# Kernel tuning notes

Hardware: AMD Instinct MI355X
Metric: run time of the kernel (lower is better)

The kernel has to match this reference:

```python
import math
import jax, jax.numpy as jnp
import numpy as np

L, NH, DF = 4, 4, 32  # num_layers, num_heads, head_dim (H=128)
EPS = 1e-5


def ln(x, g, b):
    m = x.mean(-1, keepdims=True)
    v = ((x - m) ** 2).mean(-1, keepdims=True)
    return (x - m) * jax.lax.rsqrt(v + EPS) * g + b


def mha(x, w_in, b_in, w_out, b_out):
    # torch nn.MultiheadAttention self-attention, batch_first, no mask
    B, S, H = x.shape
    q, k, v = jnp.split(x @ w_in + b_in, 3, axis=-1)
    q = q.reshape(B, S, NH, DF)
    k = k.reshape(B, S, NH, DF)
    v = v.reshape(B, S, NH, DF)
    s = jnp.einsum('bqhd,bkhd->bhqk', q, k) / math.sqrt(DF)
    a = jax.nn.softmax(s, axis=-1)
    o = jnp.einsum('bhqk,bkhd->bqhd', a, v).reshape(B, S, H)
    return o @ w_out + b_out


def _forward(X_k, time_embed, step_embed, W_tr, b_tr, W_in, b_in, g_in, be_in,
             W_e, b_e, aw, ab, ow, ob, tng, tnb, f1w, f1b, f2w, f2b, fng, fnb,
             Wq, Wk, Wv, Wo, bo, Wem, bem, Wea, bea, e1w, e1b, e2w, e2b,
             gng, gnb, eng, enb, W_out, b_out, k_index, edge_index):
    B, N, T1, Cin = X_k.shape
    H = W_in.shape[1]
    # --- precompute_graph: self-loops + structural edge features ---
    loop = jnp.arange(N, dtype=edge_index.dtype)
    ei = jnp.concatenate([edge_index, jnp.stack([loop, loop])], axis=1)
    dst, src = ei[0], ei[1]
    E = ei.shape[1]
    deg = jnp.zeros((N,), jnp.float32).at[dst].add(1.0)
    deg_max = jnp.maximum(deg.max(), 1.0)
    edge_w = 1.0 / jnp.maximum(deg[dst], 1.0)
    feat = jnp.stack([edge_w, deg[src] / deg_max, deg[dst] / deg_max], axis=1)  # [E,3]
    # --- input embedding ---
    t_emb = time_embed  # [T1, te] (lookup of arange(T1) = whole table)
    X = jnp.concatenate(
        [X_k, jnp.broadcast_to(t_emb[None, None], (B, N, T1, t_emb.shape[-1]))], axis=-1)
    h = ln(X @ W_in + b_in, g_in, be_in)
    h = h + step_embed[k_index][:, None, None, :]
    e = feat @ W_e + b_e                       # [E, de]
    t_re = t_emb @ W_tr + b_tr                 # [T1, H]
    BT = B * T1
    for l in range(L):
        # temporal attention over T1
        h_flat = h.reshape(B * N, T1, H)
        attn_out = mha(h_flat, aw[l], ab[l], ow[l], ob[l])
        h = ln(h + attn_out.reshape(B, N, T1, H), tng[l], tnb[l])
        ffn = jax.nn.gelu(h @ f1w[l] + f1b[l], approximate=False) @ f2w[l] + f2b[l]
        h = ln(h + ffn, fng[l], fnb[l])
        h = h + t_re[None, None]
        # DiGress GT sparse graph block over N
        h_BT = h.transpose(0, 2, 1, 3).reshape(BT, N, H)
        Q = (h_BT @ Wq[l]).reshape(BT, N, NH, DF)
        K = (h_BT @ Wk[l]).reshape(BT, N, NH, DF)
        V = (h_BT @ Wv[l]).reshape(BT, N, NH, DF)
        scores = (Q[:, dst] * K[:, src]).sum(-1) / math.sqrt(DF)  # [BT,E,NH]
        scores = scores * (e @ Wem[l] + bem[l] + 1.0) + (e @ Wea[l] + bea[l])
        s_max = jax.lax.stop_gradient(scores.max(axis=1, keepdims=True))
        exp_s = jnp.exp(scores - s_max)
        denom = jnp.zeros((BT, N, NH), exp_s.dtype).at[:, dst, :].add(exp_s)
        attn = exp_s / (denom[:, dst, :] + 1e-9)
        agg = (attn[..., None] * V[:, src]).reshape(BT, E, H)
        out = jnp.zeros((BT, N, H), h.dtype).at[:, dst, :].add(agg)
        h_BT = h_BT + out @ Wo[l] + bo[l]
        h_mean = jax.lax.stop_gradient(h_BT).mean(0)               # [N,H]
        e_in = jnp.concatenate([h_mean[dst], h_mean[src], e], axis=-1)
        e_mlp = jax.nn.gelu(e_in @ e1w[l] + e1b[l], approximate=False) @ e2w[l] + e2b[l]
        e = ln(e + e_mlp, eng[l], enb[l])
        h = ln(h_BT.reshape(B, T1, N, H).transpose(0, 2, 1, 3), gng[l], gnb[l])
    return jax.nn.softmax(h @ W_out + b_out, axis=-1)


def setup_inputs() -> dict:
    key = jax.random.key(0)
    B, N, T1 = 2, 2000, 12
    sd, cc, te, H, de, nh = 4, 2, 16, 128, 16, 4
    Cin = (1 + cc) * sd  # 12
    E0, max_steps = 32000, 1024
    ks = iter(jax.random.split(key, 60))
    def rn(*shape, s=0.05):
        return jax.random.normal(next(ks), shape, jnp.float32) * s
    z = lambda *s: jnp.zeros(s, jnp.float32)
    o = lambda *s: jnp.ones(s, jnp.float32)
    return dict(
        X_k=jax.random.normal(next(ks), (B, N, T1, Cin), jnp.float32),
        time_embed=rn(T1, te), step_embed=rn(max_steps, H),
        W_tr=rn(te, H), b_tr=z(H),
        W_in=rn(Cin + te, H), b_in=z(H), g_in=o(H), be_in=z(H),
        W_e=rn(3, de), b_e=z(de),
        aw=rn(L, H, 3 * H), ab=z(L, 3 * H), ow=rn(L, H, H), ob=z(L, H),
        tng=o(L, H), tnb=z(L, H),
        f1w=rn(L, H, 2 * H), f1b=z(L, 2 * H), f2w=rn(L, 2 * H, H), f2b=z(L, H),
        fng=o(L, H), fnb=z(L, H),
        Wq=rn(L, H, H), Wk=rn(L, H, H), Wv=rn(L, H, H),
        Wo=rn(L, H, H), bo=z(L, H),
        Wem=rn(L, de, nh), bem=z(L, nh), Wea=rn(L, de, nh), bea=z(L, nh),
        e1w=rn(L, 2 * H + de, 4 * de), e1b=z(L, 4 * de),
        e2w=rn(L, 4 * de, de), e2b=z(L, de),
        gng=o(L, H), gnb=z(L, H), eng=o(L, de), enb=z(L, de),
        W_out=rn(H, sd), b_out=z(sd),
        k_index=jax.random.randint(next(ks), (B,), 0, max_steps),
        edge_index=jax.random.randint(next(ks), (2, E0), 0, N),
    )


def reference(X_k, time_embed, step_embed, W_tr, b_tr, W_in, b_in, g_in, be_in,
              W_e, b_e, aw, ab, ow, ob, tng, tnb, f1w, f1b, f2w, f2b, fng, fnb,
              Wq, Wk, Wv, Wo, bo, Wem, bem, Wea, bea, e1w, e1b, e2w, e2b,
              gng, gnb, eng, enb, W_out, b_out, k_index, edge_index):
    return _forward(X_k, time_embed, step_embed, W_tr, b_tr, W_in, b_in, g_in, be_in,
                    W_e, b_e, aw, ab, ow, ob, tng, tnb, f1w, f1b, f2w, f2b, fng, fnb,
                    Wq, Wk, Wv, Wo, bo, Wem, bem, Wea, bea, e1w, e1b, e2w, e2b,
                    gng, gnb, eng, enb, W_out, b_out, k_index, edge_index)
```

## Files before the change

kernel.cpp:

```cpp
#include <hip/hip_runtime.h>
#include <math.h>

#define NN 2000
#define T1C 12
#define BBC 2
#define HHC 128
#define NHD 4
#define DFD 32
#define LLC 4
#define DEC 16
#define TEC 16
#define CINC 12
#define E0C 32000
#define EEC 34000
#define BTC 24
#define MROWS 48000
#define EPSLN 1e-5f
#define SCALEQK 0.17677669529663687f

typedef __attribute__((ext_vector_type(8))) short short8;
typedef __attribute__((ext_vector_type(4))) float f32x4;


__device__ __forceinline__ unsigned short f2b(float f)
{
    unsigned u = __float_as_uint(f);
    return (unsigned short)((u + 0x7FFF + ((u >> 16) & 1)) >> 16);
}

__device__ __forceinline__ float b2f(unsigned short h)
{
    return __uint_as_float(((unsigned)h) << 16);
}


__global__ __launch_bounds__(256) void convwp_k(const float* __restrict__ W, unsigned short* __restrict__ Bp,
                                                int LN_, int K, int N, int noff, int Ntot)
{
    int idx = blockIdx.x * blockDim.x + threadIdx.x;
    int total = LN_ * K * N;
    if (idx >= total) return;
    int l = idx / (K * N);
    int r = idx - l * (K * N);
    int k = r / N;
    int n = r - k * N + noff;
    size_t off = (size_t)l * K * Ntot +
                 ((size_t)((n >> 4) * (K >> 5) + (k >> 5)) << 9) +
                 (((k >> 3) & 3) << 7) + ((n & 15) << 3) + (k & 7);
    Bp[off] = f2b(W[idx]);
}

__global__ __launch_bounds__(256) void convw12_k(const float* __restrict__ e1w, unsigned short* __restrict__ W12P)
{
    int idx = blockIdx.x * blockDim.x + threadIdx.x;
    if (idx >= LLC * 128 * 128) return;
    int l = idx >> 14;
    int r = idx & 16383;
    int c = r >> 7, k = r & 127;
    int sk = (c < 64) ? k : k + 128;
    int sc = c & 63;
    W12P[idx] = f2b(e1w[((size_t)l * 272 + sk) * 64 + sc]);
}

__global__ __launch_bounds__(256) void convwoT_k(const float* __restrict__ Wo, unsigned short* __restrict__ WoT)
{
    int idx = blockIdx.x * blockDim.x + threadIdx.x;
    if (idx >= LLC * 128 * 128) return;
    int l = idx >> 14;
    int r = idx & 16383;
    int c = r >> 7, k = r & 127;
    WoT[idx] = f2b(Wo[((size_t)l * 128 + k) * 128 + c]);
}


template<int K, int EPI, int OUTM>
__global__ __launch_bounds__(256) void gemm2_k(
    const unsigned short* __restrict__ A, const unsigned short* __restrict__ Bp,
    const float* __restrict__ bias, float* __restrict__ C, unsigned short* __restrict__ Cb,
    const float* __restrict__ res, const float* __restrict__ gam, const float* __restrict__ bet,
    const float* __restrict__ trep,
    int M, int Ntot)
{
    __shared__ unsigned short A_s[128 * 16 * 8];
    __shared__ float red2[2][128][2];

    int tid = threadIdx.x;
    int w = tid >> 6, lane = tid & 63;
    int wr = w & 1, wc = w >> 1;
    int quad = lane >> 4, lr = lane & 15;

    const unsigned short* abase = A + (size_t)blockIdx.x * 128 * K;
    int ntg0 = blockIdx.y * 8 + wc * 4;

    f32x4 acc[4][4];
#pragma unroll
    for (int mt = 0; mt < 4; mt++)
#pragma unroll
        for (int nt = 0; nt < 4; nt++) acc[mt][nt] = (f32x4){0.f, 0.f, 0.f, 0.f};

#pragma unroll
    for (int kb = 0; kb < K; kb += 128) {
        if (kb) __syncthreads();
#pragma unroll
        for (int j = 0; j < 8; j++) {
            int s = j * 256 + tid;
            int row = s >> 4, ks = s & 15;
            int ko = ks ^ (row & 15);
            uint4 d = *(const uint4*)(abase + (size_t)row * K + kb + ko * 8);
            *(uint4*)(A_s + s * 8) = d;
        }
        __syncthreads();
#pragma unroll
        for (int k0 = 0; k0 < 128; k0 += 32) {
            short8 af[4], bf[4];
#pragma unroll
            for (int mt = 0; mt < 4; mt++) {
                int row_l = wr * 64 + mt * 16 + lr;
                int koct = (k0 >> 3) + quad;
                int slot = row_l * 16 + (koct ^ lr);
                af[mt] = *(const short8*)(A_s + slot * 8);
            }
#pragma unroll
            for (int nt = 0; nt < 4; nt++) {
                size_t off = ((size_t)(ntg0 + nt) * (K >> 5) + ((kb + k0) >> 5)) * 512 + lane * 8;
                bf[nt] = *(const short8*)(Bp + off);
            }
#pragma unroll
            for (int mt = 0; mt < 4; mt++)
#pragma unroll
                for (int nt = 0; nt < 4; nt++)
                    acc[mt][nt] = __builtin_amdgcn_mfma_f32_16x16x32_bf16(af[mt], bf[nt], acc[mt][nt], 0, 0, 0);
        }
    }

    int rbase = blockIdx.x * 128 + wr * 64;
    int cbase = blockIdx.y * 128 + wc * 64;

    if constexpr (EPI != 3 && EPI != 4 && EPI != 5) {
#pragma unroll
        for (int mt = 0; mt < 4; mt++) {
#pragma unroll
            for (int nt = 0; nt < 4; nt++) {
                int colg = cbase + nt * 16 + lr;
                float bv = bias ? bias[colg] : 0.f;
#pragma unroll
                for (int i = 0; i < 4; i++) {
                    int row = rbase + mt * 16 + quad * 4 + i;
                    float x = acc[mt][nt][i] + bv;
                    if constexpr (EPI == 1) x = 0.5f * x * (1.f + erff(x * 0.70710678118654752f));
                    if constexpr (EPI == 2) x = res[(size_t)row * Ntot + colg] + x;
                    if constexpr (OUTM & 1) C[(size_t)row * Ntot + colg] = x;
                    if constexpr (OUTM & 4)
                        Cb[(size_t)blockIdx.y * M * 128 + (size_t)row * 128 + (wc * 64 + nt * 16 + lr)] = f2b(x);
                    else if constexpr (OUTM & 2)
                        Cb[(size_t)row * Ntot + colg] = f2b(x);
                }
            }
        }
    } else {
        float s[4][4], s2l[4][4];
#pragma unroll
        for (int mt = 0; mt < 4; mt++)
#pragma unroll
            for (int i = 0; i < 4; i++) { s[mt][i] = 0.f; s2l[mt][i] = 0.f; }
#pragma unroll
        for (int mt = 0; mt < 4; mt++) {
#pragma unroll
            for (int nt = 0; nt < 4; nt++) {
                int colg = cbase + nt * 16 + lr;
                float bv = bias[colg];
#pragma unroll
                for (int i = 0; i < 4; i++) {
                    int row = rbase + mt * 16 + quad * 4 + i;
                    float x = acc[mt][nt][i] + bv + res[(size_t)row * 128 + colg];
                    acc[mt][nt][i] = x;
                    s[mt][i] += x;
                    s2l[mt][i] += x * x;
                }
            }
        }
#pragma unroll
        for (int m = 1; m < 16; m <<= 1) {
#pragma unroll
            for (int mt = 0; mt < 4; mt++)
#pragma unroll
                for (int i = 0; i < 4; i++) {
                    s[mt][i]  += __shfl_xor(s[mt][i], m, 64);
                    s2l[mt][i] += __shfl_xor(s2l[mt][i], m, 64);
                }
        }
        if (lr == 0) {
#pragma unroll
            for (int mt = 0; mt < 4; mt++)
#pragma unroll
                for (int i = 0; i < 4; i++) {
                    int rl = wr * 64 + mt * 16 + quad * 4 + i;
                    red2[wc][rl][0] = s[mt][i];
                    red2[wc][rl][1] = s2l[mt][i];
                }
        }
        __syncthreads();
#pragma unroll
        for (int mt = 0; mt < 4; mt++) {
#pragma unroll
            for (int i = 0; i < 4; i++) {
                int rl = wr * 64 + mt * 16 + quad * 4 + i;
                float st  = red2[0][rl][0] + red2[1][rl][0];
                float s2t = red2[0][rl][1] + red2[1][rl][1];
                float mu = st * (1.f / 128.f);
                float rstd = rsqrtf(s2t * (1.f / 128.f) - mu * mu + EPSLN);
                int row = rbase + mt * 16 + quad * 4 + i;
                if constexpr (EPI == 4) {
                    int t = row % T1C;
                    int bn = row / T1C;
                    int b = bn / NN;
                    int n = bn - b * NN;
                    size_t rowp = (size_t)(b * T1C + t) * NN + n;
                    const float* trow = trep + t * HHC;
#pragma unroll
                    for (int nt = 0; nt < 4; nt++) {
                        int colg = cbase + nt * 16 + lr;
                        float y = (acc[mt][nt][i] - mu) * rstd * gam[colg] + bet[colg] + trow[colg];
                        C[rowp * 128 + colg] = y;
                        Cb[rowp * 128 + colg] = f2b(y);
                    }
                } else if constexpr (EPI == 5) {
                    int bt = row / NN, n = row - bt * NN;
                    int b = bt / T1C, t = bt - b * T1C;
                    size_t rowp = ((size_t)(b * NN + n)) * T1C + t;
#pragma unroll
                    for (int nt = 0; nt < 4; nt++) {
                        int colg = cbase + nt * 16 + lr;
                        float y = (acc[mt][nt][i] - mu) * rstd * gam[colg] + bet[colg];
                        C[rowp * 128 + colg] = y;
                        Cb[rowp * 128 + colg] = f2b(y);
                    }
                } else {
#pragma unroll
                    for (int nt = 0; nt < 4; nt++) {
                        int colg = cbase + nt * 16 + lr;
                        float y = (acc[mt][nt][i] - mu) * rstd * gam[colg] + bet[colg];
                        if constexpr (OUTM & 1) C[(size_t)row * 128 + colg] = y;
                        if constexpr (OUTM & 2) Cb[(size_t)row * 128 + colg] = f2b(y);
                    }
                }
            }
        }
    }
}

template<int K, int EPI, int OUTM>
static void run_gemm2(const unsigned short* A, const unsigned short* Bp, const float* bias,
                      float* C, unsigned short* Cb, const float* res, const float* g, const float* be,
                      const float* trep, int M, int Ntot, hipStream_t stream)
{
    dim3 grid(M / 128, Ntot / 128);
    gemm2_k<K, EPI, OUTM><<<grid, 256, 0, stream>>>(A, Bp, bias, C, Cb, res, g, be, trep, M, Ntot);
}


__global__ __launch_bounds__(256) void ffn_k(
    const unsigned short* __restrict__ A,
    const unsigned short* __restrict__ F1p,
    const unsigned short* __restrict__ F2p,
    const float* __restrict__ f1b_l, const float* __restrict__ f2b_l,
    const float* __restrict__ res,
    const float* __restrict__ gam, const float* __restrict__ bet,
    const float* __restrict__ trep,
    float* __restrict__ C, unsigned short* __restrict__ Cb)
{
    __shared__ unsigned short A_s[32 * 16 * 8];
    __shared__ unsigned short M_s[32 * 16 * 8];
    __shared__ float red2[2][32][2];

    int tid = threadIdx.x;
    int w = tid >> 6, lane = tid & 63;
    int wr = w & 1, wc = w >> 1;
    int quad = lane >> 4, lr = lane & 15;

    const unsigned short* abase = A + (size_t)blockIdx.x * 32 * 128;

#pragma unroll
    for (int j = 0; j < 2; j++) {
        int s = j * 256 + tid;
        int row = s >> 4, ks = s & 15;
        int ko = ks ^ (row & 15);
        uint4 d = *(const uint4*)(abase + (size_t)row * 128 + ko * 8);
        *(uint4*)(A_s + s * 8) = d;
    }
    __syncthreads();

    f32x4 facc[4];
#pragma unroll
    for (int nt = 0; nt < 4; nt++) facc[nt] = (f32x4){0.f, 0.f, 0.f, 0.f};

#pragma unroll
    for (int half = 0; half < 2; half++) {
        f32x4 macc[4];
#pragma unroll
        for (int nt = 0; nt < 4; nt++) macc[nt] = (f32x4){0.f, 0.f, 0.f, 0.f};
#pragma unroll
        for (int k0 = 0; k0 < 128; k0 += 32) {
            int row_l = wr * 16 + lr;
            int koct = (k0 >> 3) + quad;
            int slot = row_l * 16 + (koct ^ lr);
            short8 af = *(const short8*)(A_s + slot * 8);
            short8 bf[4];
#pragma unroll
            for (int nt = 0; nt < 4; nt++) {
                size_t off = ((size_t)(half * 8 + wc * 4 + nt) * 4 + (k0 >> 5)) * 512 + lane * 8;
                bf[nt] = *(const short8*)(F1p + off);
            }
#pragma unroll
            for (int nt = 0; nt < 4; nt++)
                macc[nt] = __builtin_amdgcn_mfma_f32_16x16x32_bf16(af, bf[nt], macc[nt], 0, 0, 0);
        }
        if (half) __syncthreads();
#pragma unroll
        for (int nt = 0; nt < 4; nt++) {
            int col = wc * 64 + nt * 16 + lr;
            float bv = f1b_l[half * 128 + col];
            int cchunk = col >> 3, celem = col & 7;
#pragma unroll
            for (int i = 0; i < 4; i++) {
                int row = wr * 16 + quad * 4 + i;
                float x = macc[nt][i] + bv;
                x = 0.5f * x * (1.f + erff(x * 0.70710678118654752f));
                int ks = cchunk ^ (row & 15);
                M_s[(row * 16 + ks) * 8 + celem] = f2b(x);
            }
        }
        __syncthreads();
#pragma unroll
        for (int k0 = 0; k0 < 128; k0 += 32) {
            int row_l = wr * 16 + lr;
            int koct = (k0 >> 3) + quad;
            int slot = row_l * 16 + (koct ^ lr);
            short8 af = *(const short8*)(M_s + slot * 8);
            short8 bf[4];
#pragma unroll
            for (int nt = 0; nt < 4; nt++) {
                size_t off = ((size_t)(wc * 4 + nt) * 8 + ((half * 128 + k0) >> 5)) * 512 + lane * 8;
                bf[nt] = *(const short8*)(F2p + off);
            }
#pragma unroll
            for (int nt = 0; nt < 4; nt++)
                facc[nt] = __builtin_amdgcn_mfma_f32_16x16x32_bf16(af, bf[nt], facc[nt], 0, 0, 0);
        }
    }

    int rbase = blockIdx.x * 32 + wr * 16;
    int cbase = wc * 64;
    float s[4], s2l[4];
#pragma unroll
    for (int i = 0; i < 4; i++) { s[i] = 0.f; s2l[i] = 0.f; }
#pragma unroll
    for (int nt = 0; nt < 4; nt++) {
        int colg = cbase + nt * 16 + lr;
        float bv = f2b_l[colg];
#pragma unroll
        for (int i = 0; i < 4; i++) {
            int row = rbase + quad * 4 + i;
            float x = facc[nt][i] + bv + res[(size_t)row * 128 + colg];
            facc[nt][i] = x;
            s[i] += x;
            s2l[i] += x * x;
        }
    }
#pragma unroll
    for (int m = 1; m < 16; m <<= 1) {
#pragma unroll
        for (int i = 0; i < 4; i++) {
            s[i]  += __shfl_xor(s[i], m, 64);
            s2l[i] += __shfl_xor(s2l[i], m, 64);
        }
    }
    if (lr == 0) {
#pragma unroll
        for (int i = 0; i < 4; i++) {
            int rl = wr * 16 + quad * 4 + i;
            red2[wc][rl][0] = s[i];
            red2[wc][rl][1] = s2l[i];
        }
    }
    __syncthreads();
#pragma unroll
    for (int i = 0; i < 4; i++) {
        int rl = wr * 16 + quad * 4 + i;
        float st  = red2[0][rl][0] + red2[1][rl][0];
        float s2t = red2[0][rl][1] + red2[1][rl][1];
        float mu = st * (1.f / 128.f);
        float rstd = rsqrtf(s2t * (1.f / 128.f) - mu * mu + EPSLN);
        int row = rbase + quad * 4 + i;
        int t = row % T1C;
        int bn = row / T1C;
        int b = bn / NN;
        int n = bn - b * NN;
        size_t rowp = (size_t)(b * T1C + t) * NN + n;
        const float* trow = trep + t * HHC;
#pragma unroll
        for (int nt = 0; nt < 4; nt++) {
            int colg = cbase + nt * 16 + lr;
            float y = (facc[nt][i] - mu) * rstd * gam[colg] + bet[colg] + trow[colg];
            C[rowp * 128 + colg] = y;
            Cb[rowp * 128 + colg] = f2b(y);
        }
    }
}


template<int NT>
__global__ __launch_bounds__(256) void gemm_mfma_k(
    const unsigned short* __restrict__ A, const unsigned short* __restrict__ WT,
    float* __restrict__ C, int M, int K)
{
    const int Nc = NT * 32;
    int tid = threadIdx.x;
    int w = tid >> 6, lane = tid & 63;
    int wr = w & 1, wc = w >> 1;
    int r0 = blockIdx.x * 32 + wr * 16;
    int c0 = wc * NT * 16;
    int lr = lane & 15;
    int kq = (lane >> 4) * 8;
    int arow = r0 + lr; if (arow >= M) arow = M - 1;
    const unsigned short* ap = A + (size_t)arow * K + kq;
    const unsigned short* wp = WT + (size_t)(c0 + lr) * K + kq;

    f32x4 acc[NT];
#pragma unroll
    for (int t = 0; t < NT; t++) acc[t] = (f32x4){0.f, 0.f, 0.f, 0.f};

    for (int k0 = 0; k0 < K; k0 += 32) {
        short8 a = *(const short8*)(ap + k0);
#pragma unroll
        for (int t = 0; t < NT; t++) {
            short8 b = *(const short8*)(wp + (size_t)t * 16 * K + k0);
            acc[t] = __builtin_amdgcn_mfma_f32_16x16x32_bf16(a, b, acc[t], 0, 0, 0);
        }
    }

    int orow0 = r0 + (lane >> 4) * 4;
#pragma unroll
    for (int t = 0; t < NT; t++) {
        int col = c0 + t * 16 + lr;
#pragma unroll
        for (int i = 0; i < 4; i++) {
            int row = orow0 + i;
            if (row < M) C[(size_t)row * Nc + col] = acc[t][i];
        }
    }
}

__global__ __launch_bounds__(256) void gemm_hm_k(
    const unsigned short* __restrict__ A, const unsigned short* __restrict__ WT,
    const float* __restrict__ mA, const float* __restrict__ bo,
    unsigned short* __restrict__ hmb, int M, int K)
{
    const int NT = 4;
    int tid = threadIdx.x;
    int w = tid >> 6, lane = tid & 63;
    int wr = w & 1, wc = w >> 1;
    int r0 = blockIdx.x * 32 + wr * 16;
    int c0 = wc * NT * 16;
    int lr = lane & 15;
    int kq = (lane >> 4) * 8;
    int arow = r0 + lr; if (arow >= M) arow = M - 1;
    const unsigned short* ap = A + (size_t)arow * K + kq;
    const unsigned short* wp = WT + (size_t)(c0 + lr) * K + kq;

    f32x4 acc[NT];
#pragma unroll
    for (int t = 0; t < NT; t++) acc[t] = (f32x4){0.f, 0.f, 0.f, 0.f};

    for (int k0 = 0; k0 < K; k0 += 32) {
        short8 a = *(const short8*)(ap + k0);
#pragma unroll
        for (int t = 0; t < NT; t++) {
            short8 b = *(const short8*)(wp + (size_t)t * 16 * K + k0);
            acc[t] = __builtin_amdgcn_mfma_f32_16x16x32_bf16(a, b, acc[t], 0, 0, 0);
        }
    }

    int orow0 = r0 + (lane >> 4) * 4;
#pragma unroll
    for (int t = 0; t < NT; t++) {
        int col = c0 + t * 16 + lr;
#pragma unroll
        for (int i = 0; i < 4; i++) {
            int row = orow0 + i;
            if (row < M) {
                float x = acc[t][i] + mA[(size_t)row * 128 + col] + bo[col];
                hmb[(size_t)row * 128 + col] = f2b(x);
            }
        }
    }
}


__global__ __launch_bounds__(256) void emlp_k(const float* __restrict__ P12,
                                              const int* __restrict__ dst, const int* __restrict__ src,
                                              const float* __restrict__ e1wE, const float* __restrict__ e1b_l,
                                              const float* __restrict__ e2w_l, const float* __restrict__ e2b_l,
                                              const float* __restrict__ g, const float* __restrict__ be,
                                              float* __restrict__ e)
{
    __shared__ float tl[4][64];
    int wv = threadIdx.x >> 6, l = threadIdx.x & 63;
    int r = blockIdx.x * 4 + wv;
    int d = dst[r], s = src[r];
    const float* ep = e + (size_t)r * DEC;
    float t = P12[(size_t)d * 128 + l] + P12[(size_t)s * 128 + 64 + l] + e1b_l[l];
#pragma unroll
    for (int k = 0; k < DEC; k++) t += ep[k] * e1wE[k * 64 + l];
    t = 0.5f * t * (1.f + erff(t * 0.70710678118654752f));
    tl[wv][l] = t;
    __syncthreads();
    int c = l & 15, kq = l >> 4;
    float p = 0.f;
#pragma unroll
    for (int j = 0; j < 16; j++) p += tl[wv][kq * 16 + j] * e2w_l[(kq * 16 + j) * 16 + c];
    p += __shfl_xor(p, 16, 64);
    p += __shfl_xor(p, 32, 64);
    float x = p + e2b_l[c] + ep[c];
    float s1 = x, s2 = x * x;
#pragma unroll
    for (int m = 1; m < 16; m <<= 1) {
        s1 += __shfl_xor(s1, m, 64);
        s2 += __shfl_xor(s2, m, 64);
    }
    float mu = s1 * (1.f / 16.f);
    float rstd = rsqrtf(s2 * (1.f / 16.f) - mu * mu + EPSLN);
    float y = (x - mu) * rstd * g[c] + be[c];
    if (l < 16) e[(size_t)r * DEC + c] = y;
}


__global__ __launch_bounds__(256) void zero_deg_k(int* __restrict__ degi)
{
    int i = blockIdx.x * blockDim.x + threadIdx.x;
    if (i < NN) degi[i] = 0;
}

__global__ __launch_bounds__(256) void build_edges_k(const int* __restrict__ eidx,
                                                     int* __restrict__ dst, int* __restrict__ src,
                                                     int* __restrict__ degi)
{
    int e = blockIdx.x * blockDim.x + threadIdx.x;
    if (e >= EEC) return;
    int d, s;
    if (e < E0C) { d = eidx[e]; s = eidx[E0C + e]; }
    else { d = e - E0C; s = e - E0C; }
    dst[e] = d;
    src[e] = s;
    atomicAdd(&degi[d], 1);
}

__global__ __launch_bounds__(256) void scan_k(const int* __restrict__ degi, int* __restrict__ rowptr,
                                              int* __restrict__ cursor, float* __restrict__ degmaxf)
{
    __shared__ int ssum[256];
    __shared__ int smx[256];
    int tid = threadIdx.x;
    int vals[8];
    int s = 0, mx = 0;
    int base = tid * 8;
#pragma unroll
    for (int j = 0; j < 8; j++) {
        int idx = base + j;
        int v = (idx < NN) ? degi[idx] : 0;
        vals[j] = v; s += v; mx = max(mx, v);
    }
    ssum[tid] = s; smx[tid] = mx;
    __syncthreads();
    for (int off = 1; off < 256; off <<= 1) {
        int t = (tid >= off) ? ssum[tid - off] : 0;
        __syncthreads();
        ssum[tid] += t;
        __syncthreads();
    }
    for (int off = 128; off > 0; off >>= 1) {
        if (tid < off) smx[tid] = max(smx[tid], smx[tid + off]);
        __syncthreads();
    }
    if (tid == 0) *degmaxf = fmaxf((float)smx[0], 1.f);
    int running = ssum[tid] - s;
#pragma unroll
    for (int j = 0; j < 8; j++) {
        int idx = base + j;
        if (idx < NN) { rowptr[idx] = running; cursor[idx] = running; running += vals[j]; }
    }
    if (tid == 255) rowptr[NN] = ssum[255];
}

__global__ __launch_bounds__(256) void feat_k(const int* __restrict__ dst, const int* __restrict__ src,
                                              const int* __restrict__ degi, const float* __restrict__ degmaxf,
                                              int* __restrict__ cursor, int* __restrict__ srcCSR,
                                              int* __restrict__ epos,
                                              const float* __restrict__ We, const float* __restrict__ bE,
                                              float* __restrict__ e)
{
    int ei = blockIdx.x * blockDim.x + threadIdx.x;
    if (ei >= EEC) return;
    int d = dst[ei], s = src[ei];
    int pos = atomicAdd(&cursor[d], 1);
    srcCSR[pos] = s;
    epos[ei] = pos;
    float dm = *degmaxf;
    float degd = (float)degi[d], degs = (float)degi[s];
    float f0 = 1.f / fmaxf(degd, 1.f);
    float f1 = degs / dm, f2 = degd / dm;
#pragma unroll
    for (int c = 0; c < DEC; c++)
        e[ei * DEC + c] = bE[c] + f0 * We[c] + f1 * We[DEC + c] + f2 * We[2 * DEC + c];
}


__global__ __launch_bounds__(256) void embed_k(const float* __restrict__ Xk, const float* __restrict__ temb,
                                               const float* __restrict__ Win, const float* __restrict__ bin,
                                               const float* __restrict__ g, const float* __restrict__ be,
                                               const float* __restrict__ stepemb, const int* __restrict__ kidx,
                                               float* __restrict__ h, unsigned short* __restrict__ hb)
{
    int row = blockIdx.x * 4 + (threadIdx.x >> 6);
    int l = threadIdx.x & 63;
    int t = row % T1C;
    int bn = row / T1C;
    int b = bn / NN;
    const float* xk = Xk + (size_t)row * CINC;
    const float* tp = temb + t * TEC;
    float acc0 = bin[l], acc1 = bin[l + 64];
#pragma unroll
    for (int k = 0; k < CINC; k++) {
        float xv = xk[k];
        acc0 += xv * Win[k * HHC + l];
        acc1 += xv * Win[k * HHC + l + 64];
    }
#pragma unroll
    for (int k = 0; k < TEC; k++) {
        float xv = tp[k];
        acc0 += xv * Win[(CINC + k) * HHC + l];
        acc1 += xv * Win[(CINC + k) * HHC + l + 64];
    }
    float s = acc0 + acc1, s2 = acc0 * acc0 + acc1 * acc1;
#pragma unroll
    for (int m = 32; m >= 1; m >>= 1) {
        s  += __shfl_xor(s, m, 64);
        s2 += __shfl_xor(s2, m, 64);
    }
    float mu = s * (1.f / 128.f);
    float rstd = rsqrtf(s2 * (1.f / 128.f) - mu * mu + EPSLN);
    const float* se = stepemb + (size_t)kidx[b] * HHC;
    float v0 = (acc0 - mu) * rstd * g[l] + be[l] + se[l];
    float v1 = (acc1 - mu) * rstd * g[l + 64] + be[l + 64] + se[l + 64];
    size_t ob = (size_t)row * HHC;
    h[ob + l] = v0;
    h[ob + l + 64] = v1;
    hb[ob + l] = f2b(v0);
    hb[ob + l + 64] = f2b(v1);
}

__global__ __launch_bounds__(128) void tre_k(const float* __restrict__ temb, const float* __restrict__ Wtr,
                                             const float* __restrict__ btr, float* __restrict__ tre)
{
    int t = blockIdx.x, c = threadIdx.x;
    float acc = btr[c];
#pragma unroll
    for (int k = 0; k < TEC; k++) acc += temb[t * TEC + k] * Wtr[k * HHC + c];
    tre[t * HHC + c] = acc;
}


__global__ __launch_bounds__(128) void temporal_attn_k(const unsigned short* __restrict__ qkvb,
                                                       unsigned short* __restrict__ outb)
{
    int bn = blockIdx.x;
    __shared__ unsigned short qkv_s[T1C][408];
    __shared__ float s[NHD][T1C][T1C];
    int tid = threadIdx.x;
    int hh = tid >> 5, lane = tid & 31;
    const unsigned short* base = qkvb + (size_t)bn * T1C * 384;
    for (int cIdx = tid; cIdx < 576; cIdx += 128) {
        uint4 d = *(const uint4*)(base + cIdx * 8);
        int t = cIdx / 48;
        int c0 = (cIdx - t * 48) * 8;
        *(uint4*)(&qkv_s[t][c0]) = d;
    }
    __syncthreads();
    for (int idx = lane; idx < T1C * T1C; idx += 32) {
        int tq = idx / T1C, tk = idx - tq * T1C;
        const unsigned* qp = (const unsigned*)&qkv_s[tq][hh * 32];
        const unsigned* kp = (const unsigned*)&qkv_s[tk][128 + hh * 32];
        float acc = 0.f;
#pragma unroll
        for (int d = 0; d < 16; d++) {
            unsigned a = qp[d], b = kp[d];
            acc += __uint_as_float(a << 16) * __uint_as_float(b << 16);
            acc += __uint_as_float(a & 0xFFFF0000u) * __uint_as_float(b & 0xFFFF0000u);
        }
        s[hh][tq][tk] = acc * SCALEQK;
    }
    __syncthreads();
    if (tid < NHD * T1C) {
        int h2 = tid / T1C, tq = tid - h2 * T1C;
        float mx = -1e30f;
#pragma unroll
        for (int j = 0; j < T1C; j++) mx = fmaxf(mx, s[h2][tq][j]);
        float sum = 0.f;
#pragma unroll
        for (int j = 0; j < T1C; j++) { float ex = __expf(s[h2][tq][j] - mx); s[h2][tq][j] = ex; sum += ex; }
        float inv = 1.f / sum;
#pragma unroll
        for (int j = 0; j < T1C; j++) s[h2][tq][j] *= inv;
    }
    __syncthreads();
    int oc = hh * 32 + lane;
#pragma unroll
    for (int t = 0; t < T1C; t++) {
        float acc = 0.f;
#pragma unroll
        for (int tk = 0; tk < T1C; tk++) acc += s[hh][t][tk] * b2f(qkv_s[tk][256 + oc]);
        outb[((size_t)bn * T1C + t) * HHC + oc] = f2b(acc);
    }
}


__global__ __launch_bounds__(256) void emea_k(const float* __restrict__ e, const int* __restrict__ epos,
                                              const float* __restrict__ Wem, const float* __restrict__ bem,
                                              const float* __restrict__ Wea, const float* __restrict__ bea,
                                              float* __restrict__ ec)
{
    int r = blockIdx.x * blockDim.x + threadIdx.x;
    if (r >= EEC) return;
    float ev[DEC];
#pragma unroll
    for (int k = 0; k < DEC; k++) ev[k] = e[r * DEC + k];
    int pos = epos[r];
#pragma unroll
    for (int hh = 0; hh < NHD; hh++) {
        float a = bem[hh], b2 = bea[hh];
#pragma unroll
        for (int k = 0; k < DEC; k++) { a += ev[k] * Wem[k * NHD + hh]; b2 += ev[k] * Wea[k * NHD + hh]; }
        ec[(size_t)pos * 8 + hh * 2]     = (a + 1.f) * SCALEQK;
        ec[(size_t)pos * 8 + hh * 2 + 1] = b2;
    }
}

__global__ __launch_bounds__(256) void sagg_k(const unsigned short* __restrict__ Q,
                                              const unsigned short* __restrict__ K,
                                              const unsigned short* __restrict__ V,
                                              const int* __restrict__ rowptr, const int* __restrict__ srcCSR,
                                              const float* __restrict__ ec, unsigned short* __restrict__ outb)
{
    int wv = threadIdx.x >> 6;
    int lane = threadIdx.x & 63;
    int blk = blockIdx.x;
    int bt = blk % BTC;
    int n  = (blk / BTC) * 4 + wv;
    int cg = lane & 15;
    int es = lane >> 4;
    int hh = cg >> 2;
    size_t base = (size_t)bt * NN;
    uint4 qd = *(const uint4*)(Q + (base + n) * HHC + cg * 8);
    unsigned qv[4] = {qd.x, qd.y, qd.z, qd.w};
    float q[8];
#pragma unroll
    for (int jj = 0; jj < 4; jj++) {
        q[2 * jj]     = __uint_as_float(qv[jj] << 16);
        q[2 * jj + 1] = __uint_as_float(qv[jj] & 0xFFFF0000u);
    }
    int s0 = rowptr[n], s1 = rowptr[n + 1];
    float acc[8];
#pragma unroll
    for (int j = 0; j < 8; j++) acc[j] = 0.f;
    float den = 0.f;
    for (int i = s0 + es; i < s1; i += 4) {
        int sn = srcCSR[i];
        uint4 kd = *(const uint4*)(K + (base + sn) * HHC + cg * 8);
        uint4 vd = *(const uint4*)(V + (base + sn) * HHC + cg * 8);
        float2 c2 = *(const float2*)(ec + (size_t)i * 8 + hh * 2);
        unsigned kv[4] = {kd.x, kd.y, kd.z, kd.w};
        float p = 0.f;
#pragma unroll
        for (int jj = 0; jj < 4; jj++) {
            p += q[2 * jj]     * __uint_as_float(kv[jj] << 16);
            p += q[2 * jj + 1] * __uint_as_float(kv[jj] & 0xFFFF0000u);
        }
        p += __shfl_xor(p, 1, 64);
        p += __shfl_xor(p, 2, 64);
        float w = __expf(p * c2.x + c2.y);
        unsigned vv[4] = {vd.x, vd.y, vd.z, vd.w};
#pragma unroll
        for (int jj = 0; jj < 4; jj++) {
            acc[2 * jj]     += w * __uint_as_float(vv[jj] << 16);
            acc[2 * jj + 1] += w * __uint_as_float(vv[jj] & 0xFFFF0000u);
        }
        den += w;
    }
#pragma unroll
    for (int j = 0; j < 8; j++) {
        acc[j] += __shfl_xor(acc[j], 16, 64);
        acc[j] += __shfl_xor(acc[j], 32, 64);
    }
    den += __shfl_xor(den, 16, 64);
    den += __shfl_xor(den, 32, 64);
    if (es == 0) {
        float inv = den + 1e-9f;
        unsigned short r[8];
#pragma unroll
        for (int j = 0; j < 8; j++) r[j] = f2b(acc[j] / inv);
        *(uint4*)(outb + (base + n) * HHC + cg * 8) = *(uint4*)r;
    }
}

__global__ __launch_bounds__(128) void hmean2_k(const float* __restrict__ hBT,
                                                const unsigned short* __restrict__ aggb,
                                                float* __restrict__ mA, unsigned short* __restrict__ mBb)
{
    int n = blockIdx.x, c = threadIdx.x;
    float sA = 0.f, sB = 0.f;
#pragma unroll
    for (int bt = 0; bt < BTC; bt++) {
        size_t off = ((size_t)bt * NN + n) * HHC + c;
        sA += hBT[off];
        sB += b2f(aggb[off]);
    }
    mA[n * HHC + c] = sA * (1.f / BTC);
    mBb[n * HHC + c] = f2b(sB * (1.f / BTC));
}


__global__ __launch_bounds__(256) void out_k(const float* __restrict__ h, const float* __restrict__ Wout,
                                             const float* __restrict__ bout, float* __restrict__ out)
{
    int row = blockIdx.x * 4 + (threadIdx.x >> 6);
    int lane = threadIdx.x & 63;
    const float* hp = h + (size_t)row * HHC;
    float x0 = hp[lane], x1 = hp[lane + 64];
    float w00 = Wout[lane * 4 + 0], w01 = Wout[lane * 4 + 1];
    float w02 = Wout[lane * 4 + 2], w03 = Wout[lane * 4 + 3];
    float w10 = Wout[(lane + 64) * 4 + 0], w11 = Wout[(lane + 64) * 4 + 1];
    float w12 = Wout[(lane + 64) * 4 + 2], w13 = Wout[(lane + 64) * 4 + 3];
    float p0 = x0 * w00 + x1 * w10;
    float p1 = x0 * w01 + x1 * w11;
    float p2 = x0 * w02 + x1 * w12;
    float p3 = x0 * w03 + x1 * w13;
#pragma unroll
    for (int m = 32; m >= 1; m >>= 1) {
        p0 += __shfl_xor(p0, m, 64);
        p1 += __shfl_xor(p1, m, 64);
        p2 += __shfl_xor(p2, m, 64);
        p3 += __shfl_xor(p3, m, 64);
    }
    if (lane == 0) {
        float l0 = p0 + bout[0], l1 = p1 + bout[1], l2 = p2 + bout[2], l3 = p3 + bout[3];
        float mx = fmaxf(fmaxf(l0, l1), fmaxf(l2, l3));
        float e0 = __expf(l0 - mx), e1 = __expf(l1 - mx), e2 = __expf(l2 - mx), e3 = __expf(l3 - mx);
        float inv = 1.f / (e0 + e1 + e2 + e3);
        float4 o = {e0 * inv, e1 * inv, e2 * inv, e3 * inv};
        *(float4*)(out + (size_t)row * 4) = o;
    }
}


extern "C" void kernel_launch(void* const* d_in, const int* in_sizes, int n_in,
                              void* d_out, int out_size, void* d_ws, size_t ws_size,
                              hipStream_t stream)
{
    const float* Xk      = (const float*)d_in[0];
    const float* temb    = (const float*)d_in[1];
    const float* stepemb = (const float*)d_in[2];
    const float* Wtr     = (const float*)d_in[3];
    const float* btr     = (const float*)d_in[4];
    const float* Win     = (const float*)d_in[5];
    const float* bin     = (const float*)d_in[6];
    const float* gin     = (const float*)d_in[7];
    const float* bein    = (const float*)d_in[8];
    const float* We      = (const float*)d_in[9];
    const float* bE      = (const float*)d_in[10];
    const float* aw      = (const float*)d_in[11];
    const float* ab      = (const float*)d_in[12];
    const float* ow      = (const float*)d_in[13];
    const float* ob      = (const float*)d_in[14];
    const float* tng     = (const float*)d_in[15];
    const float* tnb     = (const float*)d_in[16];
    const float* f1w     = (const float*)d_in[17];
    const float* f1b     = (const float*)d_in[18];
    const float* f2w     = (const float*)d_in[19];
    const float* f2b_    = (const float*)d_in[20];
    const float* fng     = (const float*)d_in[21];
    const float* fnb     = (const float*)d_in[22];
    const float* Wq      = (const float*)d_in[23];
    const float* Wk      = (const float*)d_in[24];
    const float* Wv      = (const float*)d_in[25];
    const float* Wo      = (const float*)d_in[26];
    const float* bo      = (const float*)d_in[27];
    const float* Wem     = (const float*)d_in[28];
    const float* bem     = (const float*)d_in[29];
    const float* Wea     = (const float*)d_in[30];
    const float* bea     = (const float*)d_in[31];
    const float* e1w     = (const float*)d_in[32];
    const float* e1b     = (const float*)d_in[33];
    const float* e2w     = (const float*)d_in[34];
    const float* e2b     = (const float*)d_in[35];
    const float* gng     = (const float*)d_in[36];
    const float* gnb     = (const float*)d_in[37];
    const float* eng     = (const float*)d_in[38];
    const float* enb     = (const float*)d_in[39];
    const float* Wout    = (const float*)d_in[40];
    const float* bout    = (const float*)d_in[41];
    const int*   kidx    = (const int*)d_in[42];
    const int*   eidx    = (const int*)d_in[43];
    float* outp = (float*)d_out;

    char* wsp = (char*)d_ws;
    auto alloc = [&](size_t nbytes) -> void* {
        void* p = (void*)wsp;
        wsp += (nbytes + 255) & ~(size_t)255;
        return p;
    };
    float* h     = (float*)alloc((size_t)MROWS * HHC * 4);
    unsigned short* hb = (unsigned short*)alloc((size_t)MROWS * HHC * 2);
    float* hBT   = (float*)alloc((size_t)MROWS * HHC * 4);
    unsigned short* hBTb = (unsigned short*)alloc((size_t)MROWS * HHC * 2);
    float* bufC  = (float*)alloc((size_t)MROWS * 384 * 4);
    unsigned short* bufDb = (unsigned short*)alloc((size_t)MROWS * HHC * 2);
    float* ebuf  = (float*)alloc((size_t)EEC * DEC * 4);
    float* ec    = (float*)alloc((size_t)EEC * NHD * 2 * 4);
    float* P12   = (float*)alloc((size_t)NN * HHC * 4);
    float* mA    = (float*)alloc((size_t)NN * HHC * 4);
    unsigned short* mBb = (unsigned short*)alloc((size_t)NN * HHC * 2);
    unsigned short* hmb = (unsigned short*)alloc((size_t)NN * HHC * 2);
    float* tre   = (float*)alloc((size_t)T1C * HHC * 4);
    float* degmaxf = (float*)alloc(4);
    int* degi   = (int*)alloc((size_t)NN * 4);
    int* dst    = (int*)alloc((size_t)EEC * 4);
    int* srcA   = (int*)alloc((size_t)EEC * 4);
    int* srcCSR = (int*)alloc((size_t)EEC * 4);
    int* epos   = (int*)alloc((size_t)EEC * 4);
    int* rowptr = (int*)alloc((size_t)(NN + 1) * 4);
    int* cursor = (int*)alloc((size_t)NN * 4);
    unsigned short* awP   = (unsigned short*)alloc((size_t)LLC * 384 * 128 * 2);
    unsigned short* owP   = (unsigned short*)alloc((size_t)LLC * 128 * 128 * 2);
    unsigned short* f1P   = (unsigned short*)alloc((size_t)LLC * 256 * 128 * 2);
    unsigned short* f2P   = (unsigned short*)alloc((size_t)LLC * 128 * 256 * 2);
    unsigned short* WqkvP = (unsigned short*)alloc((size_t)LLC * 384 * 128 * 2);
    unsigned short* WoP   = (unsigned short*)alloc((size_t)LLC * 128 * 128 * 2);
    unsigned short* WoT   = (unsigned short*)alloc((size_t)LLC * 128 * 128 * 2);
    unsigned short* W12P  = (unsigned short*)alloc((size_t)LLC * 128 * 128 * 2);

    unsigned short* bufCb = (unsigned short*)bufC;
    unsigned short* Qc    = (unsigned short*)bufC;
    unsigned short* Kc    = Qc + (size_t)MROWS * HHC;
    unsigned short* Vc    = Kc + (size_t)MROWS * HHC;

    {
        auto cwp = [&](const float* W, unsigned short* Bp, int K, int N, int noff, int Ntot) {
            int total = LLC * K * N;
            convwp_k<<<(total + 255) / 256, 256, 0, stream>>>(W, Bp, LLC, K, N, noff, Ntot);
        };
        cwp(aw,  awP, 128, 384, 0, 384);
        cwp(ow,  owP, 128, 128, 0, 128);
        cwp(f1w, f1P, 128, 256, 0, 256);
        cwp(f2w, f2P, 256, 128, 0, 128);
        cwp(Wq,  WqkvP, 128, 128, 0,   384);
        cwp(Wk,  WqkvP, 128, 128, 128, 384);
        cwp(Wv,  WqkvP, 128, 128, 256, 384);
        cwp(Wo,  WoP, 128, 128, 0, 128);
        convwoT_k<<<(LLC * 128 * 128 + 255) / 256, 256, 0, stream>>>(Wo, WoT);
        convw12_k<<<(LLC * 128 * 128 + 255) / 256, 256, 0, stream>>>(e1w, W12P);
    }

    zero_deg_k<<<(NN + 255) / 256, 256, 0, stream>>>(degi);
    build_edges_k<<<(EEC + 255) / 256, 256, 0, stream>>>(eidx, dst, srcA, degi);
    scan_k<<<1, 256, 0, stream>>>(degi, rowptr, cursor, degmaxf);
    feat_k<<<(EEC + 255) / 256, 256, 0, stream>>>(dst, srcA, degi, degmaxf, cursor, srcCSR, epos, We, bE, ebuf);

    embed_k<<<MROWS / 4, 256, 0, stream>>>(Xk, temb, Win, bin, gin, bein, stepemb, kidx, h, hb);
    tre_k<<<T1C, 128, 0, stream>>>(temb, Wtr, btr, tre);

    for (int l = 0; l < LLC; l++) {
        const unsigned short* awP_l   = awP   + (size_t)l * 384 * 128;
        const unsigned short* owP_l   = owP   + (size_t)l * 128 * 128;
        const unsigned short* f1P_l   = f1P   + (size_t)l * 256 * 128;
        const unsigned short* f2P_l   = f2P   + (size_t)l * 128 * 256;
        const unsigned short* WqkvP_l = WqkvP + (size_t)l * 384 * 128;
        const unsigned short* WoP_l   = WoP   + (size_t)l * 128 * 128;
        const unsigned short* WoT_l   = WoT   + (size_t)l * 128 * 128;
        const unsigned short* W12P_l  = W12P  + (size_t)l * 128 * 128;
        const float* ab_l  = ab  + (size_t)l * 3 * HHC;
        const float* ob_l  = ob  + (size_t)l * HHC;
        const float* tng_l = tng + (size_t)l * HHC;
        const float* tnb_l = tnb + (size_t)l * HHC;
        const float* f1b_l = f1b + (size_t)l * 256;
        const float* f2b_l = f2b_ + (size_t)l * HHC;
        const float* fng_l = fng + (size_t)l * HHC;
        const float* fnb_l = fnb + (size_t)l * HHC;
        const float* bo_l  = bo  + (size_t)l * HHC;
        const float* Wem_l = Wem + (size_t)l * DEC * NHD;
        const float* bem_l = bem + (size_t)l * NHD;
        const float* Wea_l = Wea + (size_t)l * DEC * NHD;
        const float* bea_l = bea + (size_t)l * NHD;
        const float* e1wE_l = e1w + ((size_t)l * 272 + 256) * 64;
        const float* e1b_l = e1b + (size_t)l * 64;
        const float* e2w_l = e2w + (size_t)l * 64 * DEC;
        const float* e2b_l = e2b + (size_t)l * DEC;
        const float* gng_l = gng + (size_t)l * HHC;
        const float* gnb_l = gnb + (size_t)l * HHC;
        const float* eng_l = eng + (size_t)l * DEC;
        const float* enb_l = enb + (size_t)l * DEC;

        run_gemm2<128, 0, 2>(hb, awP_l, ab_l, nullptr, bufCb, nullptr, nullptr, nullptr, nullptr, MROWS, 384, stream);
        temporal_attn_k<<<BBC * NN, 128, 0, stream>>>(bufCb, bufDb);
        run_gemm2<128, 3, 3>(bufDb, owP_l, ob_l, h, hb, h, tng_l, tnb_l, nullptr, MROWS, 128, stream);
        ffn_k<<<MROWS / 32, 256, 0, stream>>>(hb, f1P_l, f2P_l, f1b_l, f2b_l, h,
                                              fng_l, fnb_l, tre, hBT, hBTb);
        run_gemm2<128, 0, 4>(hBTb, WqkvP_l, nullptr, nullptr, Qc, nullptr, nullptr, nullptr, nullptr, MROWS, 384, stream);
        emea_k<<<(EEC + 255) / 256, 256, 0, stream>>>(ebuf, epos, Wem_l, bem_l, Wea_l, bea_l, ec);
        sagg_k<<<BTC * (NN / 4), 256, 0, stream>>>(Qc, Kc, Vc, rowptr, srcCSR, ec, bufDb);
        hmean2_k<<<NN, 128, 0, stream>>>(hBT, bufDb, mA, mBb);
        run_gemm2<128, 5, 3>(bufDb, WoP_l, bo_l, h, hb, hBT, gng_l, gnb_l, nullptr, MROWS, 128, stream);
        gemm_hm_k<<<(NN + 31) / 32, 256, 0, stream>>>(mBb, WoT_l, mA, bo_l, hmb, NN, 128);
        gemm_mfma_k<4><<<(NN + 31) / 32, 256, 0, stream>>>(hmb, W12P_l, P12, NN, 128);
        emlp_k<<<EEC / 4, 256, 0, stream>>>(P12, dst, srcA, e1wE_l, e1b_l, e2w_l, e2b_l, eng_l, enb_l, ebuf);
    }

    out_k<<<MROWS / 4, 256, 0, stream>>>(h, Wout, bout, outp);
}
```

Baseline: 1.032 ms.

## Fuse attention out-projection and LayerNorm into the FFN kernel

```diff
diff --git a/kernel.cpp b/kernel.cpp
--- a/kernel.cpp
+++ b/kernel.cpp
@@ -259,13 +259,16 @@
 }
 
 
-__global__ __launch_bounds__(256) void ffn_k(
+__global__ __launch_bounds__(256) void offn_k(
     const unsigned short* __restrict__ A,
+    const unsigned short* __restrict__ Wp,
+    const float* __restrict__ ob_l,
+    const float* __restrict__ resh,
+    const float* __restrict__ tng_l, const float* __restrict__ tnb_l,
     const unsigned short* __restrict__ F1p,
     const unsigned short* __restrict__ F2p,
     const float* __restrict__ f1b_l, const float* __restrict__ f2b_l,
-    const float* __restrict__ res,
-    const float* __restrict__ gam, const float* __restrict__ bet,
+    const float* __restrict__ fng_l, const float* __restrict__ fnb_l,
     const float* __restrict__ trep,
     float* __restrict__ C, unsigned short* __restrict__ Cb)
 {
@@ -290,6 +293,85 @@
     }
     __syncthreads();
 
+    f32x4 wacc[4];
+#pragma unroll
+    for (int nt = 0; nt < 4; nt++) wacc[nt] = (f32x4){0.f, 0.f, 0.f, 0.f};
+#pragma unroll
+    for (int k0 = 0; k0 < 128; k0 += 32) {
+        int row_l = wr * 16 + lr;
+        int koct = (k0 >> 3) + quad;
+        int slot = row_l * 16 + (koct ^ lr);
+        short8 af = *(const short8*)(A_s + slot * 8);
+        short8 bf[4];
+#pragma unroll
+        for (int nt = 0; nt < 4; nt++) {
+            size_t off = ((size_t)(wc * 4 + nt) * 4 + (k0 >> 5)) * 512 + lane * 8;
+            bf[nt] = *(const short8*)(Wp + off);
+        }
+#pragma unroll
+        for (int nt = 0; nt < 4; nt++)
+            wacc[nt] = __builtin_amdgcn_mfma_f32_16x16x32_bf16(af, bf[nt], wacc[nt], 0, 0, 0);
+    }
+
+    int rbase = blockIdx.x * 32 + wr * 16;
+    int cbase = wc * 64;
+
+    float yv[4][4];
+    {
+        float s1[4], s2v[4];
+#pragma unroll
+        for (int i = 0; i < 4; i++) { s1[i] = 0.f; s2v[i] = 0.f; }
+#pragma unroll
+        for (int nt = 0; nt < 4; nt++) {
+            int colg = cbase + nt * 16 + lr;
+            float bv = ob_l[colg];
+#pragma unroll
+            for (int i = 0; i < 4; i++) {
+                int row = rbase + quad * 4 + i;
+                float x = wacc[nt][i] + bv + resh[(size_t)row * 128 + colg];
+                yv[nt][i] = x;
+                s1[i] += x;
+                s2v[i] += x * x;
+            }
+        }
+#pragma unroll
+        for (int m = 1; m < 16; m <<= 1) {
+#pragma unroll
+            for (int i = 0; i < 4; i++) {
+                s1[i]  += __shfl_xor(s1[i], m, 64);
+                s2v[i] += __shfl_xor(s2v[i], m, 64);
+            }
+        }
+        if (lr == 0) {
+#pragma unroll
+            for (int i = 0; i < 4; i++) {
+                int rl = wr * 16 + quad * 4 + i;
+                red2[wc][rl][0] = s1[i];
+                red2[wc][rl][1] = s2v[i];
+            }
+        }
+        __syncthreads();
+#pragma unroll
+        for (int i = 0; i < 4; i++) {
+            int rl = wr * 16 + quad * 4 + i;
+            float st  = red2[0][rl][0] + red2[1][rl][0];
+            float s2t = red2[0][rl][1] + red2[1][rl][1];
+            float mu = st * (1.f / 128.f);
+            float rstd = rsqrtf(s2t * (1.f / 128.f) - mu * mu + EPSLN);
+            int row = wr * 16 + quad * 4 + i;
+#pragma unroll
+            for (int nt = 0; nt < 4; nt++) {
+                int col = cbase + nt * 16 + lr;
+                float y = (yv[nt][i] - mu) * rstd * tng_l[col] + tnb_l[col];
+                yv[nt][i] = y;
+                int cchunk = col >> 3, celem = col & 7;
+                int ks = cchunk ^ (row & 15);
+                A_s[(row * 16 + ks) * 8 + celem] = f2b(y);
+            }
+        }
+    }
+    __syncthreads();
+
     f32x4 facc[4];
 #pragma unroll
     for (int nt = 0; nt < 4; nt++) facc[nt] = (f32x4){0.f, 0.f, 0.f, 0.f};
@@ -349,8 +431,6 @@
         }
     }
 
-    int rbase = blockIdx.x * 32 + wr * 16;
-    int cbase = wc * 64;
     float s[4], s2l[4];
 #pragma unroll
     for (int i = 0; i < 4; i++) { s[i] = 0.f; s2l[i] = 0.f; }
@@ -360,8 +440,7 @@
         float bv = f2b_l[colg];
 #pragma unroll
         for (int i = 0; i < 4; i++) {
-            int row = rbase + quad * 4 + i;
-            float x = facc[nt][i] + bv + res[(size_t)row * 128 + colg];
+            float x = facc[nt][i] + bv + yv[nt][i];
             facc[nt][i] = x;
             s[i] += x;
             s2l[i] += x * x;
@@ -401,7 +480,7 @@
 #pragma unroll
         for (int nt = 0; nt < 4; nt++) {
             int colg = cbase + nt * 16 + lr;
-            float y = (facc[nt][i] - mu) * rstd * gam[colg] + bet[colg] + trow[colg];
+            float y = (facc[nt][i] - mu) * rstd * fng_l[colg] + fnb_l[colg] + trow[colg];
             C[rowp * 128 + colg] = y;
             Cb[rowp * 128 + colg] = f2b(y);
         }
@@ -1011,9 +1090,9 @@
 
         run_gemm2<128, 0, 2>(hb, awP_l, ab_l, nullptr, bufCb, nullptr, nullptr, nullptr, nullptr, MROWS, 384, stream);
         temporal_attn_k<<<BBC * NN, 128, 0, stream>>>(bufCb, bufDb);
-        run_gemm2<128, 3, 3>(bufDb, owP_l, ob_l, h, hb, h, tng_l, tnb_l, nullptr, MROWS, 128, stream);
-        ffn_k<<<MROWS / 32, 256, 0, stream>>>(hb, f1P_l, f2P_l, f1b_l, f2b_l, h,
-                                              fng_l, fnb_l, tre, hBT, hBTb);
+        offn_k<<<MROWS / 32, 256, 0, stream>>>(bufDb, owP_l, ob_l, h, tng_l, tnb_l,
+                                               f1P_l, f2P_l, f1b_l, f2b_l, fng_l, fnb_l,
+                                               tre, hBT, hBTb);
         run_gemm2<128, 0, 4>(hBTb, WqkvP_l, nullptr, nullptr, Qc, nullptr, nullptr, nullptr, nullptr, MROWS, 384, stream);
         emea_k<<<(EEC + 255) / 256, 256, 0, stream>>>(ebuf, epos, Wem_l, bem_l, Wea_l, bea_l, ec);
         sagg_k<<<BTC * (NN / 4), 256, 0, stream>>>(Qc, Kc, Vc, rowptr, srcCSR, ec, bufDb);
```

Result: faster. 991.3 us, median of 2 (-3.9%).
